# Optimization experiments

Measured on AMD Instinct MI355X. Metric: run time of the kernel, lower is better.

Reference implementation:

```python
import jax, jax.numpy as jnp
import numpy as np

B, S, D = 1, 1024, 4096
NH, NKV, HD = 32, 8, 128
CACHE = 1024


def setup_inputs() -> dict:
    key = jax.random.key(0)
    ks = jax.random.split(key, 9)
    return {
        "hidden_states": jax.random.normal(ks[0], (B, S, D), jnp.float32),
        "freqs_cos": jax.random.uniform(ks[1], (S, HD // 2), jnp.float32),
        "freqs_sin": jax.random.uniform(ks[2], (S, HD // 2), jnp.float32),
        "atten_mask": jnp.zeros((S, CACHE + S), jnp.float32),
        "k_cache": jax.random.normal(ks[3], (B, NKV, HD, CACHE), jnp.float32),
        "v_cache": jax.random.normal(ks[4], (B, NKV, CACHE, HD), jnp.float32),
        "wq": jax.random.normal(ks[5], (NH, HD, D), jnp.float32) * 0.02,
        "wk": jax.random.normal(ks[6], (NKV, HD, D), jnp.float32) * 0.02,
        "wv": jax.random.normal(ks[7], (NKV, HD, D), jnp.float32) * 0.02,
        "wo": jax.random.normal(ks[8], (D, NH * HD), jnp.float32) * 0.02,
    }


def _rope(x, cos, sin):
    # x: [b, s, h, hd]; cos/sin: [s, hd//2]
    half = x.shape[-1] // 2
    xr, xi = x[..., :half], x[..., half:]
    c = cos[None, :, None, :]
    sn = sin[None, :, None, :]
    return jnp.concatenate([xr * c - xi * sn, xr * sn + xi * c], axis=-1)


def reference(hidden_states, freqs_cos, freqs_sin, atten_mask, k_cache, v_cache, wq, wk, wv, wo):
    b, s, d = hidden_states.shape
    nh, hd, _ = wq.shape
    nkv = wk.shape[0]
    g = nh // nkv  # query heads per KV head
    scale = float(hd) ** 0.5

    # projections (equivalent to per-head 1x1 convs)
    q = jnp.einsum("bsd,hed->bshe", hidden_states, wq)   # [b,s,nh,hd]
    k = jnp.einsum("bsd,hed->bshe", hidden_states, wk)   # [b,s,nkv,hd]
    v = jnp.einsum("bsd,hed->bshe", hidden_states, wv)   # [b,s,nkv,hd]

    q = _rope(q, freqs_cos, freqs_sin)
    k = _rope(k, freqs_cos, freqs_sin)

    # concat KV cache: kh [b,nkv,hd,KV], vh [b,nkv,KV,hd]
    kh = jnp.concatenate([k_cache, k.transpose(0, 2, 3, 1)], axis=-1)
    vh = jnp.concatenate([v_cache, v.transpose(0, 2, 1, 3)], axis=2)

    # grouped attention: head i uses kv group i // g
    qg = q.reshape(b, s, nkv, g, hd).transpose(0, 2, 3, 1, 4)  # [b,n,g,s,e]
    scores = jnp.einsum("bngse,bnet->bngst", qg, kh) / scale + atten_mask
    p = jax.nn.softmax(scores, axis=-1)
    yg = jnp.einsum("bngst,bnte->bngse", p, vh)               # [b,n,g,s,e]
    y = yg.transpose(0, 3, 1, 2, 4).reshape(b, s, nh * hd)     # head order n*g+j

    y = jnp.einsum("bsf,df->bsd", y, wo)
    return (y, kh, vh)
```

## Files before the change

### kernel.cpp

```cpp
#include <hip/hip_runtime.h>
#include <hip/hip_bf16.h>
#include <stdint.h>

#define S_LEN 1024
#define D_MODEL 4096
#define NHEAD 32
#define NKV 8
#define HD 128
#define CACHE_T 1024
#define T_TOT 2048
#define NQKV 6144
#define QSCALE 0.08838834764831845f

typedef __attribute__((ext_vector_type(8))) short short8;
typedef __attribute__((ext_vector_type(4))) float floatx4;
typedef __attribute__((ext_vector_type(16))) float floatx16;

__device__ __forceinline__ unsigned short f2bf(float f) {
  union { float f; uint32_t u; } v; v.f = f;
  uint32_t r = v.u + 0x7FFFu + ((v.u >> 16) & 1u);
  return (unsigned short)(r >> 16);
}

__device__ __forceinline__ void gload_lds16(const void* g, void* s) {
  __builtin_amdgcn_global_load_lds((const __attribute__((address_space(1))) void*)g,
                                   (__attribute__((address_space(3))) void*)s, 16, 0, 0);
}

__global__ void convf2b_kernel(const float* __restrict__ in, unsigned short* __restrict__ out, int n8) {
  int stride = gridDim.x * blockDim.x;
  for (int t = blockIdx.x * blockDim.x + threadIdx.x; t < n8; t += stride) {
    int i = t * 8;
    floatx4 a = *(const floatx4*)(in + i);
    floatx4 b = *(const floatx4*)(in + i + 4);
    short8 o;
    o[0] = (short)f2bf(a[0]); o[1] = (short)f2bf(a[1]); o[2] = (short)f2bf(a[2]); o[3] = (short)f2bf(a[3]);
    o[4] = (short)f2bf(b[0]); o[5] = (short)f2bf(b[1]); o[6] = (short)f2bf(b[2]); o[7] = (short)f2bf(b[3]);
    *(short8*)(out + i) = o;
  }
}

__global__ void mask_flag_kernel(const float* __restrict__ m, int n, int* __restrict__ flag) {
  int stride = gridDim.x * blockDim.x;
  bool nz = false;
  for (int i = blockIdx.x * blockDim.x + threadIdx.x; i < n; i += stride)
    nz |= (m[i] != 0.0f);
  if (nz) atomicOr(flag, 1);
}

__global__ __launch_bounds__(256, 3)
void gemm_bf_kernel(const unsigned short* __restrict__ A,
                    const unsigned short* __restrict__ W,
                    float* __restrict__ C,
                    int M, int N, int K, int ldc, int GM)
{
  __shared__ __align__(16) unsigned char As[2][64 * 128];
  __shared__ __align__(16) unsigned char Bs[2][128 * 128];

  const int nwg = gridDim.x;
  int orig = blockIdx.x;
  int wg = (orig & 7) * (nwg >> 3) + (orig >> 3);
  const int mt = wg % GM, nt = wg / GM;
  const int m0 = mt * 64, n0 = nt * 128;

  const int tid = threadIdx.x;
  const int wid = tid >> 6, lane = tid & 63;
  const int g4 = lane >> 4, r16 = lane & 15;
  const int wr = (wid >> 1) * 32, wc = (wid & 1) * 64;

  const int lr = lane >> 3, lc = lane & 7;
  const unsigned short* Arow[2];
  const unsigned short* Wrow[4];
#pragma unroll
  for (int i = 0; i < 2; ++i) {
    int r = (wid * 2 + i) * 8 + lr;
    Arow[i] = A + (size_t)(m0 + r) * K + (lc ^ (r & 7)) * 8;
  }
#pragma unroll
  for (int i = 0; i < 4; ++i) {
    int r = (wid * 4 + i) * 8 + lr;
    Wrow[i] = W + (size_t)(n0 + r) * K + (lc ^ (r & 7)) * 8;
  }

  auto stage = [&](int buf, int kt) {
    const int kb = kt * 64;
#pragma unroll
    for (int i = 0; i < 2; ++i)
      gload_lds16(Arow[i] + kb, &As[buf][(wid * 2 + i) * 1024]);
#pragma unroll
    for (int i = 0; i < 4; ++i)
      gload_lds16(Wrow[i] + kb, &Bs[buf][(wid * 4 + i) * 1024]);
  };

  floatx4 acc[2][4];
#pragma unroll
  for (int m = 0; m < 2; ++m)
#pragma unroll
    for (int n = 0; n < 4; ++n) acc[m][n] = (floatx4){0.f, 0.f, 0.f, 0.f};

  const int NK = K >> 6;
  stage(0, 0);
  __syncthreads();
  int cur = 0;
  for (int kt = 0; kt < NK; ++kt) {
    if (kt + 1 < NK) stage(cur ^ 1, kt + 1);
#pragma unroll
    for (int kk = 0; kk < 2; ++kk) {
      const int kb = kk * 64 + g4 * 16;
      short8 af[2], bf[4];
#pragma unroll
      for (int m = 0; m < 2; ++m) {
        int row = wr + m * 16 + r16;
        af[m] = *(const short8*)(&As[cur][row * 128 + (kb ^ ((row & 7) << 4))]);
      }
#pragma unroll
      for (int n = 0; n < 4; ++n) {
        int row = wc + n * 16 + r16;
        bf[n] = *(const short8*)(&Bs[cur][row * 128 + (kb ^ ((row & 7) << 4))]);
      }
#pragma unroll
      for (int m = 0; m < 2; ++m)
#pragma unroll
        for (int n = 0; n < 4; ++n)
          acc[m][n] = __builtin_amdgcn_mfma_f32_16x16x32_bf16(af[m], bf[n], acc[m][n], 0, 0, 0);
    }
    __syncthreads();
    cur ^= 1;
  }

#pragma unroll
  for (int m = 0; m < 2; ++m)
#pragma unroll
    for (int n = 0; n < 4; ++n)
#pragma unroll
      for (int j = 0; j < 4; ++j)
        C[(size_t)(m0 + wr + m * 16 + g4 * 4 + j) * ldc + (n0 + wc + n * 16 + r16)] = acc[m][n][j];
}

__global__ __launch_bounds__(256, 2)
void gemm_kernel(const unsigned short* __restrict__ A,
                 const float* __restrict__ W0, const float* __restrict__ W1, const float* __restrict__ W2,
                 int n1, int n2,
                 float* __restrict__ C,
                 int M, int N, int K, int GM)
{
  __shared__ __align__(16) unsigned char As[2][128 * 128];
  __shared__ __align__(16) unsigned char Bs[2][128 * 128];

  const int nwg = gridDim.x;
  int orig = blockIdx.x;
  int xcd = orig & 7, loc = orig >> 3;
  int q = nwg >> 3, r = nwg & 7;
  int wg = (xcd < r ? xcd * (q + 1) : r * (q + 1) + (xcd - r) * q) + loc;
  const int mt = wg % GM, nt = wg / GM;
  const int m0 = mt * 128, n0 = nt * 128;

  const int tid = threadIdx.x;
  const int wid = tid >> 6, lane = tid & 63;
  const int g4 = lane >> 4, r16 = lane & 15;
  const int wr = (wid >> 1) * 64, wc = (wid & 1) * 64;

  int srow[4], skc[4];
  const float* wptr[4];
#pragma unroll
  for (int i = 0; i < 4; ++i) {
    int c = tid + 256 * i;
    srow[i] = c >> 3; skc[i] = c & 7;
    int ng = n0 + srow[i];
    wptr[i] = (ng < n1) ? (W0 + (size_t)ng * K)
            : (ng < n2) ? (W1 + (size_t)(ng - n1) * K)
                        : (W2 + (size_t)(ng - n2) * K);
  }

  short8 ar[4]; floatx4 br[8];
  auto load_tile = [&](int kt) {
    int kb = kt * 64;
#pragma unroll
    for (int i = 0; i < 4; ++i) {
      ar[i] = *(const short8*)(A + (size_t)(m0 + srow[i]) * K + kb + skc[i] * 8);
      br[2 * i]     = *(const floatx4*)(wptr[i] + kb + skc[i] * 8);
      br[2 * i + 1] = *(const floatx4*)(wptr[i] + kb + skc[i] * 8 + 4);
    }
  };
  auto write_tile = [&](int buf) {
#pragma unroll
    for (int i = 0; i < 4; ++i) {
      int off = srow[i] * 128 + ((skc[i] * 16) ^ ((srow[i] & 7) << 4));
      *(short8*)(&As[buf][off]) = ar[i];
      short8 bb;
      bb[0] = (short)f2bf(br[2 * i][0]);     bb[1] = (short)f2bf(br[2 * i][1]);
      bb[2] = (short)f2bf(br[2 * i][2]);     bb[3] = (short)f2bf(br[2 * i][3]);
      bb[4] = (short)f2bf(br[2 * i + 1][0]); bb[5] = (short)f2bf(br[2 * i + 1][1]);
      bb[6] = (short)f2bf(br[2 * i + 1][2]); bb[7] = (short)f2bf(br[2 * i + 1][3]);
      *(short8*)(&Bs[buf][off]) = bb;
    }
  };

  floatx4 acc[4][4];
#pragma unroll
  for (int m = 0; m < 4; ++m)
#pragma unroll
    for (int n = 0; n < 4; ++n) acc[m][n] = (floatx4){0.f, 0.f, 0.f, 0.f};

  const int NK = K >> 6;
  load_tile(0);
  write_tile(0);
  __syncthreads();
  int cur = 0;
  for (int kt = 0; kt < NK; ++kt) {
    if (kt + 1 < NK) load_tile(kt + 1);
#pragma unroll
    for (int kk = 0; kk < 2; ++kk) {
      const int kb = kk * 32 + g4 * 8;
      short8 af[4], bfr[4];
#pragma unroll
      for (int m = 0; m < 4; ++m) {
        int row = wr + m * 16 + r16;
        af[m] = *(const short8*)(&As[cur][row * 128 + ((kb * 2) ^ ((row & 7) << 4))]);
      }
#pragma unroll
      for (int n = 0; n < 4; ++n) {
        int row = wc + n * 16 + r16;
        bfr[n] = *(const short8*)(&Bs[cur][row * 128 + ((kb * 2) ^ ((row & 7) << 4))]);
      }
#pragma unroll
      for (int m = 0; m < 4; ++m)
#pragma unroll
        for (int n = 0; n < 4; ++n)
          acc[m][n] = __builtin_amdgcn_mfma_f32_16x16x32_bf16(af[m], bfr[n], acc[m][n], 0, 0, 0);
    }
    if (kt + 1 < NK) write_tile(cur ^ 1);
    __syncthreads();
    cur ^= 1;
  }

#pragma unroll
  for (int m = 0; m < 4; ++m)
#pragma unroll
    for (int n = 0; n < 4; ++n)
#pragma unroll
      for (int j = 0; j < 4; ++j)
        C[(size_t)(m0 + wr + m * 16 + g4 * 4 + j) * N + (n0 + wc + n * 16 + r16)] = acc[m][n][j];
}

__global__ void rope_q_kernel(const float* __restrict__ qkv, const float* __restrict__ fc,
                              const float* __restrict__ fs, unsigned short* __restrict__ qb)
{
  const int s = blockIdx.x, t = threadIdx.x;
  const int head = t >> 3, e0 = (t & 7) * 8;
  const float* base = qkv + (size_t)s * NQKV + head * HD + e0;
  floatx4 xr0 = *(const floatx4*)(base);
  floatx4 xr1 = *(const floatx4*)(base + 4);
  floatx4 xi0 = *(const floatx4*)(base + 64);
  floatx4 xi1 = *(const floatx4*)(base + 68);
  floatx4 c0 = *(const floatx4*)(fc + s * 64 + e0);
  floatx4 c1 = *(const floatx4*)(fc + s * 64 + e0 + 4);
  floatx4 s0 = *(const floatx4*)(fs + s * 64 + e0);
  floatx4 s1 = *(const floatx4*)(fs + s * 64 + e0 + 4);
  short8 outr, outi;
#pragma unroll
  for (int j = 0; j < 4; ++j) {
    outr[j]     = (short)f2bf((xr0[j] * c0[j] - xi0[j] * s0[j]) * QSCALE);
    outr[4 + j] = (short)f2bf((xr1[j] * c1[j] - xi1[j] * s1[j]) * QSCALE);
    outi[j]     = (short)f2bf((xr0[j] * s0[j] + xi0[j] * c0[j]) * QSCALE);
    outi[4 + j] = (short)f2bf((xr1[j] * s1[j] + xi1[j] * c1[j]) * QSCALE);
  }
  unsigned short* ob = qb + (size_t)s * D_MODEL + head * HD + e0;
  *(short8*)ob = outr;
  *(short8*)(ob + 64) = outi;
}

__global__ void rope_k_kernel(const float* __restrict__ qkv, const float* __restrict__ fc,
                              const float* __restrict__ fs, float* __restrict__ kh,
                              unsigned short* __restrict__ khb)
{
  __shared__ float T[128][65];
  const int n = blockIdx.x >> 4, s0 = (blockIdx.x & 15) * 64;
  const int tid = threadIdx.x;
  const int sl = tid >> 2, e0 = (tid & 3) * 16;
  const int s = s0 + sl;
  const float* base = qkv + (size_t)s * NQKV + D_MODEL + n * HD;
  float xr[16], xi[16], cc[16], sn[16];
#pragma unroll
  for (int i = 0; i < 16; i += 4) {
    *(floatx4*)(xr + i) = *(const floatx4*)(base + e0 + i);
    *(floatx4*)(xi + i) = *(const floatx4*)(base + 64 + e0 + i);
    *(floatx4*)(cc + i) = *(const floatx4*)(fc + s * 64 + e0 + i);
    *(floatx4*)(sn + i) = *(const floatx4*)(fs + s * 64 + e0 + i);
  }
  short8 r0, r1, i0, i1;
#pragma unroll
  for (int i = 0; i < 16; ++i) {
    float vr = xr[i] * cc[i] - xi[i] * sn[i];
    float vi = xr[i] * sn[i] + xi[i] * cc[i];
    T[e0 + i][sl] = vr;
    T[64 + e0 + i][sl] = vi;
    unsigned short br = f2bf(vr), bi = f2bf(vi);
    if (i < 8) { r0[i] = (short)br; i0[i] = (short)bi; }
    else       { r1[i - 8] = (short)br; i1[i - 8] = (short)bi; }
  }
  unsigned short* kb = khb + ((size_t)n * T_TOT + CACHE_T + s) * HD;
  *(short8*)(kb + e0) = r0;       *(short8*)(kb + e0 + 8) = r1;
  *(short8*)(kb + 64 + e0) = i0;  *(short8*)(kb + 64 + e0 + 8) = i1;
  __syncthreads();
  const int e = tid >> 1, hf = tid & 1;
  float* dst = kh + ((size_t)n * HD + e) * T_TOT + CACHE_T + s0 + hf * 32;
#pragma unroll
  for (int i = 0; i < 32; i += 4) {
    floatx4 v;
    v[0] = T[e][hf * 32 + i]; v[1] = T[e][hf * 32 + i + 1];
    v[2] = T[e][hf * 32 + i + 2]; v[3] = T[e][hf * 32 + i + 3];
    *(floatx4*)(dst + i) = v;
  }
}

__global__ void v_scatter_kernel(const float* __restrict__ qkv, float* __restrict__ vh,
                                 unsigned short* __restrict__ vtb)
{
  __shared__ __align__(16) unsigned short T[128][72];
  const int n = blockIdx.x >> 4, s0 = (blockIdx.x & 15) * 64;
  const int tid = threadIdx.x;
  const int sl = tid >> 2, e0 = (tid & 3) * 32;
  const float* src = qkv + (size_t)(s0 + sl) * NQKV + D_MODEL + NKV * HD + n * HD + e0;
  float* dst = vh + ((size_t)n * T_TOT + CACHE_T + s0 + sl) * HD + e0;
#pragma unroll
  for (int i = 0; i < 32; i += 4) {
    floatx4 v = *(const floatx4*)(src + i);
    *(floatx4*)(dst + i) = v;
    T[e0 + i][sl] = f2bf(v[0]); T[e0 + i + 1][sl] = f2bf(v[1]);
    T[e0 + i + 2][sl] = f2bf(v[2]); T[e0 + i + 3][sl] = f2bf(v[3]);
  }
  __syncthreads();
  const int e = tid >> 1, hf = tid & 1;
  unsigned short* ob = vtb + ((size_t)n * HD + e) * T_TOT + CACHE_T + s0 + hf * 32;
#pragma unroll
  for (int i = 0; i < 32; i += 8) *(short8*)(ob + i) = *(const short8*)(&T[e][hf * 32 + i]);
}

__global__ void cache_k_kernel(const float* __restrict__ kc, float* __restrict__ kh,
                               unsigned short* __restrict__ khb)
{
  __shared__ __align__(16) unsigned short T[64][72];
  const int b = blockIdx.x;
  const int n = b >> 5, et = (b >> 4) & 1, tt = b & 15;
  const int e0 = et * 64, t0 = tt * 64;
  const int tid = threadIdx.x;
  const int el = tid >> 2, tc = (tid & 3) * 16;
  const float* src = kc + ((size_t)n * HD + e0 + el) * CACHE_T + t0 + tc;
  float* dst = kh + ((size_t)n * HD + e0 + el) * T_TOT + t0 + tc;
#pragma unroll
  for (int i = 0; i < 16; i += 4) {
    floatx4 v = *(const floatx4*)(src + i);
    *(floatx4*)(dst + i) = v;
    T[tc + i][el] = f2bf(v[0]); T[tc + i + 1][el] = f2bf(v[1]);
    T[tc + i + 2][el] = f2bf(v[2]); T[tc + i + 3][el] = f2bf(v[3]);
  }
  __syncthreads();
  const int tl = tid >> 2, ec = (tid & 3) * 16;
  unsigned short* ob = khb + ((size_t)n * T_TOT + t0 + tl) * HD + e0 + ec;
#pragma unroll
  for (int i = 0; i < 16; i += 8) *(short8*)(ob + i) = *(const short8*)(&T[tl][ec + i]);
}

__global__ void cache_v_kernel(const float* __restrict__ vc, float* __restrict__ vh,
                               unsigned short* __restrict__ vtb)
{
  __shared__ __align__(16) unsigned short T[128][72];
  const int n = blockIdx.x >> 4, t0 = (blockIdx.x & 15) * 64;
  const int tid = threadIdx.x;
  const int tl = tid >> 2, e0 = (tid & 3) * 32;
  const float* src = vc + ((size_t)n * CACHE_T + t0 + tl) * HD + e0;
  float* dst = vh + ((size_t)n * T_TOT + t0 + tl) * HD + e0;
#pragma unroll
  for (int i = 0; i < 32; i += 4) {
    floatx4 v = *(const floatx4*)(src + i);
    *(floatx4*)(dst + i) = v;
    T[e0 + i][tl] = f2bf(v[0]); T[e0 + i + 1][tl] = f2bf(v[1]);
    T[e0 + i + 2][tl] = f2bf(v[2]); T[e0 + i + 3][tl] = f2bf(v[3]);
  }
  __syncthreads();
  const int e = tid >> 1, hf = tid & 1;
  unsigned short* ob = vtb + ((size_t)n * HD + e) * T_TOT + t0 + hf * 32;
#pragma unroll
  for (int i = 0; i < 32; i += 8) *(short8*)(ob + i) = *(const short8*)(&T[e][hf * 32 + i]);
}

__global__ __launch_bounds__(256, 2)
void attn_kernel(const unsigned short* __restrict__ Qb, const unsigned short* __restrict__ Kb,
                 const unsigned short* __restrict__ Vb, const float* __restrict__ mask,
                 const int* __restrict__ flag, unsigned short* __restrict__ Ob,
                 float* __restrict__ Upart, float* __restrict__ mlpart, int nsplit)
{
  __shared__ __align__(16) unsigned char KL[2][64 * 256];
  __shared__ __align__(16) unsigned char VL[2][128 * 128];

  const int nwg = gridDim.x;
  int orig = blockIdx.x;
  int wg = (orig & 7) * (nwg >> 3) + (orig >> 3);
  const int per_n = 32 * nsplit;
  const int nkv = wg / per_n;
  const int rem = wg % per_n;
  const int kvs = rem >> 5;
  const int inner = rem & 31;
  const int h = nkv * 4 + (inner >> 3);
  const int qt = inner & 7;
  const int TKV = T_TOT / nsplit;

  const int tid = threadIdx.x, wid = tid >> 6, lane = tid & 63;
  const int l31 = lane & 31, hi = lane >> 5;
  const int qrow = qt * 128 + wid * 32 + l31;
  const bool use_mask = (*flag) != 0;

  short8 qf[8];
#pragma unroll
  for (int c = 0; c < 8; ++c)
    qf[c] = *(const short8*)(Qb + (size_t)qrow * D_MODEL + h * HD + c * 16 + hi * 8);

  floatx16 acc[4];
#pragma unroll
  for (int et = 0; et < 4; ++et)
    acc[et] = (floatx16){0.f,0.f,0.f,0.f,0.f,0.f,0.f,0.f,0.f,0.f,0.f,0.f,0.f,0.f,0.f,0.f};
  float m = -1e30f, l = 0.f;

  const unsigned short* Kbase = Kb + (size_t)nkv * T_TOT * HD + (size_t)kvs * TKV * HD;
  const unsigned short* Vbase = Vb + (size_t)nkv * HD * T_TOT + (size_t)kvs * TKV;

  const unsigned short* kp[4];
  const unsigned short* vp[4];
  int kbase_off[4], vbase_off[4];
#pragma unroll
  for (int i = 0; i < 4; ++i) {
    int krow = wid * 16 + i * 4 + (lane >> 4);
    int kch  = (lane & 15) ^ (krow & 7);
    kp[i] = Kbase + (size_t)krow * HD + kch * 8;
    kbase_off[i] = (wid * 16 + i * 4) * 256;
    int vrow = wid * 32 + i * 8 + (lane >> 3);
    int vch  = (lane & 7) ^ (vrow & 7);
    vp[i] = Vbase + (size_t)vrow * T_TOT + vch * 8;
    vbase_off[i] = (wid * 32 + i * 8) * 128;
  }

#pragma unroll
  for (int i = 0; i < 4; ++i) gload_lds16(kp[i], &KL[0][kbase_off[i]]);
#pragma unroll
  for (int i = 0; i < 4; ++i) gload_lds16(vp[i], &VL[0][vbase_off[i]]);
#pragma unroll
  for (int i = 0; i < 4; ++i) { kp[i] += 64 * HD; vp[i] += 64; }
  __syncthreads();

  int cur = 0;
  for (int t0 = 0; t0 < TKV; t0 += 64) {
    if (t0 + 64 < TKV) {
#pragma unroll
      for (int i = 0; i < 4; ++i) gload_lds16(kp[i], &KL[cur ^ 1][kbase_off[i]]);
#pragma unroll
      for (int i = 0; i < 4; ++i) gload_lds16(vp[i], &VL[cur ^ 1][vbase_off[i]]);
#pragma unroll
      for (int i = 0; i < 4; ++i) { kp[i] += 64 * HD; vp[i] += 64; }
    }

    floatx16 sc[2];
#pragma unroll
    for (int ts = 0; ts < 2; ++ts) {
      sc[ts] = (floatx16){0.f,0.f,0.f,0.f,0.f,0.f,0.f,0.f,0.f,0.f,0.f,0.f,0.f,0.f,0.f,0.f};
      const int krow = ts * 32 + l31;
      const int swz = (krow & 7) << 4;
      const unsigned char* kr = &KL[cur][krow * 256];
#pragma unroll
      for (int c = 0; c < 8; ++c) {
        short8 kf = *(const short8*)(kr + ((c * 32 + hi * 16) ^ swz));
        sc[ts] = __builtin_amdgcn_mfma_f32_32x32x16_bf16(kf, qf[c], sc[ts], 0, 0, 0);
      }
    }

    if (use_mask) {
#pragma unroll
      for (int ts = 0; ts < 2; ++ts)
#pragma unroll
        for (int r = 0; r < 16; ++r) {
          int tg = kvs * TKV + t0 + ts * 32 + (r & 3) + 8 * (r >> 2) + 4 * hi;
          sc[ts][r] += mask[(size_t)qrow * T_TOT + tg];
        }
    }

    float pm = sc[0][0];
#pragma unroll
    for (int r = 1; r < 16; ++r) pm = fmaxf(pm, sc[0][r]);
#pragma unroll
    for (int r = 0; r < 16; ++r) pm = fmaxf(pm, sc[1][r]);
    pm = fmaxf(pm, __shfl_xor(pm, 32));

    if (__any(pm > m + 8.f)) {
      float nm = fmaxf(m, pm);
      float corr = __expf(m - nm);
      m = nm; l *= corr;
#pragma unroll
      for (int r = 0; r < 16; ++r) {
        float cr = __shfl(corr, (r & 3) + 8 * (r >> 2) + 4 * hi);
#pragma unroll
        for (int et = 0; et < 4; ++et) acc[et][r] *= cr;
      }
    }

    unsigned cpk[4][4];
    float ls = 0.f;
#pragma unroll
    for (int ts = 0; ts < 2; ++ts)
#pragma unroll
      for (int i = 0; i < 8; ++i) {
        float plo = __expf(sc[ts][2 * i] - m);
        float phi = __expf(sc[ts][2 * i + 1] - m);
        ls += plo + phi;
        union { __hip_bfloat162 h2; unsigned u; } cv;
        cv.h2 = __float22bfloat162_rn(make_float2(plo, phi));
        cpk[ts * 2 + (i >> 2)][i & 3] = cv.u;
      }
    ls += __shfl_xor(ls, 32);
    l += ls;

    short8 pa[4];
#pragma unroll
    for (int tc = 0; tc < 4; ++tc) {
      unsigned s0 = (unsigned)__shfl_xor((int)cpk[tc][0], 32);
      unsigned s1 = (unsigned)__shfl_xor((int)cpk[tc][1], 32);
      unsigned s2 = (unsigned)__shfl_xor((int)cpk[tc][2], 32);
      unsigned s3 = (unsigned)__shfl_xor((int)cpk[tc][3], 32);
      union { unsigned u[4]; short8 v; } fr;
      fr.u[0] = hi ? s2 : cpk[tc][0];
      fr.u[1] = hi ? s3 : cpk[tc][1];
      fr.u[2] = hi ? cpk[tc][2] : s0;
      fr.u[3] = hi ? cpk[tc][3] : s1;
      pa[tc] = fr.v;
    }

#pragma unroll
    for (int et = 0; et < 4; ++et) {
      const int vrow = et * 32 + l31;
      const int swz = (vrow & 7) << 4;
      const unsigned char* vr = &VL[cur][vrow * 128];
#pragma unroll
      for (int tc = 0; tc < 4; ++tc) {
        short8 vf = *(const short8*)(vr + ((tc * 32 + hi * 16) ^ swz));
        acc[et] = __builtin_amdgcn_mfma_f32_32x32x16_bf16(pa[tc], vf, acc[et], 0, 0, 0);
      }
    }
    __syncthreads();
    cur ^= 1;
  }

  if (nsplit == 2) {
    float* Ub = Upart + (size_t)kvs * (NHEAD * S_LEN) * HD;
#pragma unroll
    for (int et = 0; et < 4; ++et)
#pragma unroll
      for (int r = 0; r < 16; ++r) {
        int q = qt * 128 + wid * 32 + (r & 3) + 8 * (r >> 2) + 4 * hi;
        Ub[((size_t)h * S_LEN + q) * HD + et * 32 + l31] = acc[et][r];
      }
    if (lane < 32) {
      float* mlp = mlpart + ((size_t)kvs * (NHEAD * S_LEN) + (size_t)h * S_LEN + qrow) * 2;
      mlp[0] = m; mlp[1] = l;
    }
  } else {
    float inv = 1.0f / l;
#pragma unroll
    for (int et = 0; et < 4; ++et)
#pragma unroll
      for (int r = 0; r < 16; ++r) {
        float ir = __shfl(inv, (r & 3) + 8 * (r >> 2) + 4 * hi);
        int q = qt * 128 + wid * 32 + (r & 3) + 8 * (r >> 2) + 4 * hi;
        Ob[(size_t)q * D_MODEL + h * HD + et * 32 + l31] = f2bf(acc[et][r] * ir);
      }
  }
}

__global__ void attn_combine_kernel(const float* __restrict__ U, const float* __restrict__ ml,
                                    unsigned short* __restrict__ Ob)
{
  const int t = blockIdx.x * 256 + threadIdx.x;
  const int r = t >> 4;
  const int e0 = (t & 15) * 8;
  const float m1 = ml[(size_t)r * 2],                     l1 = ml[(size_t)r * 2 + 1];
  const float m2 = ml[((size_t)(NHEAD * S_LEN) + r) * 2], l2 = ml[((size_t)(NHEAD * S_LEN) + r) * 2 + 1];
  const float M = fmaxf(m1, m2);
  const float a1 = __expf(m1 - M), a2 = __expf(m2 - M);
  const float inv = 1.0f / (l1 * a1 + l2 * a2);
  const float* u1 = U + (size_t)r * HD + e0;
  const float* u2 = U + (size_t)(NHEAD * S_LEN) * HD + (size_t)r * HD + e0;
  floatx4 x1a = *(const floatx4*)u1, x1b = *(const floatx4*)(u1 + 4);
  floatx4 x2a = *(const floatx4*)u2, x2b = *(const floatx4*)(u2 + 4);
  const int s = r & (S_LEN - 1), hh = r >> 10;
  unsigned short* ob = Ob + (size_t)s * D_MODEL + hh * HD + e0;
  short8 o;
#pragma unroll
  for (int k = 0; k < 4; ++k) {
    o[k]     = (short)f2bf((x1a[k] * a1 + x2a[k] * a2) * inv);
    o[4 + k] = (short)f2bf((x1b[k] * a1 + x2b[k] * a2) * inv);
  }
  *(short8*)ob = o;
}

extern "C" void kernel_launch(void* const* d_in, const int* in_sizes, int n_in,
                              void* d_out, int out_size, void* d_ws, size_t ws_size,
                              hipStream_t stream)
{
  const float* hs   = (const float*)d_in[0];
  const float* fc   = (const float*)d_in[1];
  const float* fs   = (const float*)d_in[2];
  const float* mask = (const float*)d_in[3];
  const float* kc   = (const float*)d_in[4];
  const float* vc   = (const float*)d_in[5];
  const float* wq   = (const float*)d_in[6];
  const float* wk   = (const float*)d_in[7];
  const float* wv   = (const float*)d_in[8];
  const float* wo   = (const float*)d_in[9];

  float* y  = (float*)d_out;
  float* kh = y + (size_t)S_LEN * D_MODEL;
  float* vh = kh + (size_t)NKV * HD * T_TOT;

  char* ws = (char*)d_ws;
  unsigned short* hs_b   = (unsigned short*)ws;
  float* qkv             = (float*)(ws + 8388608u);
  unsigned short* attn_o = (unsigned short*)(ws + 8388608u);
  unsigned short* khb    = (unsigned short*)(ws + 33554432u);
  unsigned short* vtb    = (unsigned short*)(ws + 37748736u);
  int* flag              = (int*)(ws + 41943040u);
  unsigned short* slotW  = (unsigned short*)(ws + 41943296u);

  const size_t base = 41943296ull;
  const bool big = ws_size >= base + 50331648ull;
  const bool mid = ws_size >= base + 33554432ull;
  const int nsplit = (ws_size >= base + 34078720ull) ? 2 : 1;
  float* Upart  = (float*)(ws + base);
  float* mlpart = (float*)(ws + base + 33554432u);

  hipMemsetAsync(flag, 0, 4, stream);
  mask_flag_kernel<<<256, 256, 0, stream>>>(mask, S_LEN * T_TOT, flag);
  convf2b_kernel<<<2048, 256, 0, stream>>>(hs, hs_b, S_LEN * D_MODEL / 8);

  if (big) {
    convf2b_kernel<<<2048, 256, 0, stream>>>(wq, slotW, NHEAD * HD * D_MODEL / 8);
    convf2b_kernel<<<2048, 256, 0, stream>>>(wk, slotW + (size_t)4096 * 4096, NKV * HD * D_MODEL / 8);
    convf2b_kernel<<<2048, 256, 0, stream>>>(wv, slotW + (size_t)5120 * 4096, NKV * HD * D_MODEL / 8);
    gemm_bf_kernel<<<768, 256, 0, stream>>>(hs_b, slotW, qkv, 1024, 6144, 4096, 6144, 16);
  } else if (mid) {
    convf2b_kernel<<<2048, 256, 0, stream>>>(wk, slotW, NKV * HD * D_MODEL / 8);
    convf2b_kernel<<<2048, 256, 0, stream>>>(wv, slotW + (size_t)1024 * 4096, NKV * HD * D_MODEL / 8);
    gemm_bf_kernel<<<256, 256, 0, stream>>>(hs_b, slotW, qkv + 4096, 1024, 2048, 4096, 6144, 16);
    convf2b_kernel<<<2048, 256, 0, stream>>>(wq, slotW, NHEAD * HD * D_MODEL / 8);
    gemm_bf_kernel<<<512, 256, 0, stream>>>(hs_b, slotW, qkv, 1024, 4096, 4096, 6144, 16);
  } else {
    gemm_kernel<<<384, 256, 0, stream>>>(hs_b, wq, wk, wv, 4096, 5120, qkv, 1024, 6144, 4096, 8);
  }

  rope_q_kernel<<<1024, 256, 0, stream>>>(qkv, fc, fs, hs_b);
  rope_k_kernel<<<128, 256, 0, stream>>>(qkv, fc, fs, kh, khb);
  v_scatter_kernel<<<128, 256, 0, stream>>>(qkv, vh, vtb);
  cache_k_kernel<<<256, 256, 0, stream>>>(kc, kh, khb);
  cache_v_kernel<<<128, 256, 0, stream>>>(vc, vh, vtb);

  attn_kernel<<<256 * nsplit, 256, 0, stream>>>(hs_b, khb, vtb, mask, flag, attn_o,
                                                Upart, mlpart, nsplit);
  if (nsplit == 2)
    attn_combine_kernel<<<2048, 256, 0, stream>>>(Upart, mlpart, attn_o);

  if (mid) {
    convf2b_kernel<<<2048, 256, 0, stream>>>(wo, slotW, D_MODEL * D_MODEL / 8);
    gemm_bf_kernel<<<512, 256, 0, stream>>>(attn_o, slotW, y, 1024, 4096, 4096, 4096, 16);
  } else {
    gemm_kernel<<<256, 256, 0, stream>>>(attn_o, wo, wo, wo, 1 << 29, 1 << 29, y, 1024, 4096, 4096, 8);
  }
}
```

Baseline: 264.4 us.

## Fuse fp32-to-bf16 weight conversion into 64x128 GEMM loads, drop separate convert passes

The separate convf2b passes over the QKV and output-projection weights are removed. A single 64x128-tile GEMM now reads fp32 weights into registers, converts them to bf16, and writes them to LDS after the MFMA loop, prefetching one tile ahead. This avoids writing and re-reading bf16 weight copies in the workspace and cuts kernel launches. In exchange, each weight tile is loaded as fp32 and converted in-kernel by every M-tile that uses it, and register pressure rises under the 3-waves launch bound.

```diff
diff --git a/kernel.cpp b/kernel.cpp
--- a/kernel.cpp
+++ b/kernel.cpp
@@ -20,6 +20,12 @@
   union { float f; uint32_t u; } v; v.f = f;
   uint32_t r = v.u + 0x7FFFu + ((v.u >> 16) & 1u);
   return (unsigned short)(r >> 16);
+}
+
+__device__ __forceinline__ unsigned pack2bf(float a, float b) {
+  union { __hip_bfloat162 h2; unsigned u; } c;
+  c.h2 = __float22bfloat162_rn(make_float2(a, b));
+  return c.u;
 }
 
 __device__ __forceinline__ void gload_lds16(const void* g, void* s) {
@@ -49,10 +55,11 @@
 }
 
 __global__ __launch_bounds__(256, 3)
-void gemm_bf_kernel(const unsigned short* __restrict__ A,
-                    const unsigned short* __restrict__ W,
-                    float* __restrict__ C,
-                    int M, int N, int K, int ldc, int GM)
+void gemm_bfw_kernel(const unsigned short* __restrict__ A,
+                     const float* __restrict__ W0, const float* __restrict__ W1, const float* __restrict__ W2,
+                     int n1, int n2,
+                     float* __restrict__ C,
+                     int M, int N, int K, int ldc, int GM)
 {
   __shared__ __align__(16) unsigned char As[2][64 * 128];
   __shared__ __align__(16) unsigned char Bs[2][128 * 128];
@@ -70,27 +77,38 @@
 
   const int lr = lane >> 3, lc = lane & 7;
   const unsigned short* Arow[2];
-  const unsigned short* Wrow[4];
 #pragma unroll
   for (int i = 0; i < 2; ++i) {
     int r = (wid * 2 + i) * 8 + lr;
     Arow[i] = A + (size_t)(m0 + r) * K + (lc ^ (r & 7)) * 8;
   }
-#pragma unroll
-  for (int i = 0; i < 4; ++i) {
-    int r = (wid * 4 + i) * 8 + lr;
-    Wrow[i] = W + (size_t)(n0 + r) * K + (lc ^ (r & 7)) * 8;
-  }
-
-  auto stage = [&](int buf, int kt) {
-    const int kb = kt * 64;
-#pragma unroll
-    for (int i = 0; i < 2; ++i)
-      gload_lds16(Arow[i] + kb, &As[buf][(wid * 2 + i) * 1024]);
-#pragma unroll
-    for (int i = 0; i < 4; ++i)
-      gload_lds16(Wrow[i] + kb, &Bs[buf][(wid * 4 + i) * 1024]);
+
+  const int wrow = tid >> 1, wch = tid & 1;
+  const int ng = n0 + wrow;
+  const float* wptr = (ng < n1) ? (W0 + (size_t)ng * K)
+                    : (ng < n2) ? (W1 + (size_t)(ng - n1) * K)
+                                : (W2 + (size_t)(ng - n2) * K);
+  wptr += wch * 32;
+
+  floatx4 wreg[8];
+  auto wload = [&](int kt) {
+    const float* p = wptr + kt * 64;
+#pragma unroll
+    for (int i = 0; i < 8; ++i) wreg[i] = *(const floatx4*)(p + i * 4);
   };
+  auto wwrite = [&](int buf) {
+    unsigned char* dst = &Bs[buf][wrow * 128];
+    const int sw = (wrow & 7) << 4;
+#pragma unroll
+    for (int q = 0; q < 4; ++q) {
+      union { unsigned u[4]; short8 v; } pk;
+      pk.u[0] = pack2bf(wreg[2 * q][0], wreg[2 * q][1]);
+      pk.u[1] = pack2bf(wreg[2 * q][2], wreg[2 * q][3]);
+      pk.u[2] = pack2bf(wreg[2 * q + 1][0], wreg[2 * q + 1][1]);
+      pk.u[3] = pack2bf(wreg[2 * q + 1][2], wreg[2 * q + 1][3]);
+      *(short8*)(dst + ((wch * 64 + q * 16) ^ sw)) = pk.v;
+    }
+  };
 
   floatx4 acc[2][4];
 #pragma unroll
@@ -99,11 +117,20 @@
     for (int n = 0; n < 4; ++n) acc[m][n] = (floatx4){0.f, 0.f, 0.f, 0.f};
 
   const int NK = K >> 6;
-  stage(0, 0);
+  wload(0);
+#pragma unroll
+  for (int i = 0; i < 2; ++i) gload_lds16(Arow[i], &As[0][(wid * 2 + i) * 1024]);
+  wwrite(0);
   __syncthreads();
+
   int cur = 0;
   for (int kt = 0; kt < NK; ++kt) {
-    if (kt + 1 < NK) stage(cur ^ 1, kt + 1);
+    if (kt + 1 < NK) {
+      wload(kt + 1);
+#pragma unroll
+      for (int i = 0; i < 2; ++i)
+        gload_lds16(Arow[i] + (kt + 1) * 64, &As[cur ^ 1][(wid * 2 + i) * 1024]);
+    }
 #pragma unroll
     for (int kk = 0; kk < 2; ++kk) {
       const int kb = kk * 64 + g4 * 16;
@@ -124,6 +151,7 @@
         for (int n = 0; n < 4; ++n)
           acc[m][n] = __builtin_amdgcn_mfma_f32_16x16x32_bf16(af[m], bf[n], acc[m][n], 0, 0, 0);
     }
+    if (kt + 1 < NK) wwrite(cur ^ 1);
     __syncthreads();
     cur ^= 1;
   }
@@ -135,112 +163,6 @@
 #pragma unroll
       for (int j = 0; j < 4; ++j)
         C[(size_t)(m0 + wr + m * 16 + g4 * 4 + j) * ldc + (n0 + wc + n * 16 + r16)] = acc[m][n][j];
-}
-
-__global__ __launch_bounds__(256, 2)
-void gemm_kernel(const unsigned short* __restrict__ A,
-                 const float* __restrict__ W0, const float* __restrict__ W1, const float* __restrict__ W2,
-                 int n1, int n2,
-                 float* __restrict__ C,
-                 int M, int N, int K, int GM)
-{
-  __shared__ __align__(16) unsigned char As[2][128 * 128];
-  __shared__ __align__(16) unsigned char Bs[2][128 * 128];
-
-  const int nwg = gridDim.x;
-  int orig = blockIdx.x;
-  int xcd = orig & 7, loc = orig >> 3;
-  int q = nwg >> 3, r = nwg & 7;
-  int wg = (xcd < r ? xcd * (q + 1) : r * (q + 1) + (xcd - r) * q) + loc;
-  const int mt = wg % GM, nt = wg / GM;
-  const int m0 = mt * 128, n0 = nt * 128;
-
-  const int tid = threadIdx.x;
-  const int wid = tid >> 6, lane = tid & 63;
-  const int g4 = lane >> 4, r16 = lane & 15;
-  const int wr = (wid >> 1) * 64, wc = (wid & 1) * 64;
-
-  int srow[4], skc[4];
-  const float* wptr[4];
-#pragma unroll
-  for (int i = 0; i < 4; ++i) {
-    int c = tid + 256 * i;
-    srow[i] = c >> 3; skc[i] = c & 7;
-    int ng = n0 + srow[i];
-    wptr[i] = (ng < n1) ? (W0 + (size_t)ng * K)
-            : (ng < n2) ? (W1 + (size_t)(ng - n1) * K)
-                        : (W2 + (size_t)(ng - n2) * K);
-  }
-
-  short8 ar[4]; floatx4 br[8];
-  auto load_tile = [&](int kt) {
-    int kb = kt * 64;
-#pragma unroll
-    for (int i = 0; i < 4; ++i) {
-      ar[i] = *(const short8*)(A + (size_t)(m0 + srow[i]) * K + kb + skc[i] * 8);
-      br[2 * i]     = *(const floatx4*)(wptr[i] + kb + skc[i] * 8);
-      br[2 * i + 1] = *(const floatx4*)(wptr[i] + kb + skc[i] * 8 + 4);
-    }
-  };
-  auto write_tile = [&](int buf) {
-#pragma unroll
-    for (int i = 0; i < 4; ++i) {
-      int off = srow[i] * 128 + ((skc[i] * 16) ^ ((srow[i] & 7) << 4));
-      *(short8*)(&As[buf][off]) = ar[i];
-      short8 bb;
-      bb[0] = (short)f2bf(br[2 * i][0]);     bb[1] = (short)f2bf(br[2 * i][1]);
-      bb[2] = (short)f2bf(br[2 * i][2]);     bb[3] = (short)f2bf(br[2 * i][3]);
-      bb[4] = (short)f2bf(br[2 * i + 1][0]); bb[5] = (short)f2bf(br[2 * i + 1][1]);
-      bb[6] = (short)f2bf(br[2 * i + 1][2]); bb[7] = (short)f2bf(br[2 * i + 1][3]);
-      *(short8*)(&Bs[buf][off]) = bb;
-    }
-  };
-
-  floatx4 acc[4][4];
-#pragma unroll
-  for (int m = 0; m < 4; ++m)
-#pragma unroll
-    for (int n = 0; n < 4; ++n) acc[m][n] = (floatx4){0.f, 0.f, 0.f, 0.f};
-
-  const int NK = K >> 6;
-  load_tile(0);
-  write_tile(0);
-  __syncthreads();
-  int cur = 0;
-  for (int kt = 0; kt < NK; ++kt) {
-    if (kt + 1 < NK) load_tile(kt + 1);
-#pragma unroll
-    for (int kk = 0; kk < 2; ++kk) {
-      const int kb = kk * 32 + g4 * 8;
-      short8 af[4], bfr[4];
-#pragma unroll
-      for (int m = 0; m < 4; ++m) {
-        int row = wr + m * 16 + r16;
-        af[m] = *(const short8*)(&As[cur][row * 128 + ((kb * 2) ^ ((row & 7) << 4))]);
-      }
-#pragma unroll
-      for (int n = 0; n < 4; ++n) {
-        int row = wc + n * 16 + r16;
-        bfr[n] = *(const short8*)(&Bs[cur][row * 128 + ((kb * 2) ^ ((row & 7) << 4))]);
-      }
-#pragma unroll
-      for (int m = 0; m < 4; ++m)
-#pragma unroll
-        for (int n = 0; n < 4; ++n)
-          acc[m][n] = __builtin_amdgcn_mfma_f32_16x16x32_bf16(af[m], bfr[n], acc[m][n], 0, 0, 0);
-    }
-    if (kt + 1 < NK) write_tile(cur ^ 1);
-    __syncthreads();
-    cur ^= 1;
-  }
-
-#pragma unroll
-  for (int m = 0; m < 4; ++m)
-#pragma unroll
-    for (int n = 0; n < 4; ++n)
-#pragma unroll
-      for (int j = 0; j < 4; ++j)
-        C[(size_t)(m0 + wr + m * 16 + g4 * 4 + j) * N + (n0 + wc + n * 16 + r16)] = acc[m][n][j];
 }
 
 __global__ void rope_q_kernel(const float* __restrict__ qkv, const float* __restrict__ fc,
@@ -511,9 +433,7 @@
         float plo = __expf(sc[ts][2 * i] - m);
         float phi = __expf(sc[ts][2 * i + 1] - m);
         ls += plo + phi;
-        union { __hip_bfloat162 h2; unsigned u; } cv;
-        cv.h2 = __float22bfloat162_rn(make_float2(plo, phi));
-        cpk[ts * 2 + (i >> 2)][i & 3] = cv.u;
+        cpk[ts * 2 + (i >> 2)][i & 3] = pack2bf(plo, phi);
       }
     ls += __shfl_xor(ls, 32);
     l += ls;
@@ -626,11 +546,8 @@
   unsigned short* khb    = (unsigned short*)(ws + 33554432u);
   unsigned short* vtb    = (unsigned short*)(ws + 37748736u);
   int* flag              = (int*)(ws + 41943040u);
-  unsigned short* slotW  = (unsigned short*)(ws + 41943296u);
 
   const size_t base = 41943296ull;
-  const bool big = ws_size >= base + 50331648ull;
-  const bool mid = ws_size >= base + 33554432ull;
   const int nsplit = (ws_size >= base + 34078720ull) ? 2 : 1;
   float* Upart  = (float*)(ws + base);
   float* mlpart = (float*)(ws + base + 33554432u);
@@ -639,20 +556,8 @@
   mask_flag_kernel<<<256, 256, 0, stream>>>(mask, S_LEN * T_TOT, flag);
   convf2b_kernel<<<2048, 256, 0, stream>>>(hs, hs_b, S_LEN * D_MODEL / 8);
 
-  if (big) {
-    convf2b_kernel<<<2048, 256, 0, stream>>>(wq, slotW, NHEAD * HD * D_MODEL / 8);
-    convf2b_kernel<<<2048, 256, 0, stream>>>(wk, slotW + (size_t)4096 * 4096, NKV * HD * D_MODEL / 8);
-    convf2b_kernel<<<2048, 256, 0, stream>>>(wv, slotW + (size_t)5120 * 4096, NKV * HD * D_MODEL / 8);
-    gemm_bf_kernel<<<768, 256, 0, stream>>>(hs_b, slotW, qkv, 1024, 6144, 4096, 6144, 16);
-  } else if (mid) {
-    convf2b_kernel<<<2048, 256, 0, stream>>>(wk, slotW, NKV * HD * D_MODEL / 8);
-    convf2b_kernel<<<2048, 256, 0, stream>>>(wv, slotW + (size_t)1024 * 4096, NKV * HD * D_MODEL / 8);
-    gemm_bf_kernel<<<256, 256, 0, stream>>>(hs_b, slotW, qkv + 4096, 1024, 2048, 4096, 6144, 16);
-    convf2b_kernel<<<2048, 256, 0, stream>>>(wq, slotW, NHEAD * HD * D_MODEL / 8);
-    gemm_bf_kernel<<<512, 256, 0, stream>>>(hs_b, slotW, qkv, 1024, 4096, 4096, 6144, 16);
-  } else {
-    gemm_kernel<<<384, 256, 0, stream>>>(hs_b, wq, wk, wv, 4096, 5120, qkv, 1024, 6144, 4096, 8);
-  }
+  gemm_bfw_kernel<<<768, 256, 0, stream>>>(hs_b, wq, wk, wv, 4096, 5120, qkv,
+                                           1024, 6144, 4096, 6144, 16);
 
   rope_q_kernel<<<1024, 256, 0, stream>>>(qkv, fc, fs, hs_b);
   rope_k_kernel<<<128, 256, 0, stream>>>(qkv, fc, fs, kh, khb);
@@ -665,10 +570,6 @@
   if (nsplit == 2)
     attn_combine_kernel<<<2048, 256, 0, stream>>>(Upart, mlpart, attn_o);
 
-  if (mid) {
-    convf2b_kernel<<<2048, 256, 0, stream>>>(wo, slotW, D_MODEL * D_MODEL / 8);
-    gemm_bf_kernel<<<512, 256, 0, stream>>>(attn_o, slotW, y, 1024, 4096, 4096, 4096, 16);
-  } else {
-    gemm_kernel<<<256, 256, 0, stream>>>(attn_o, wo, wo, wo, 1 << 29, 1 << 29, y, 1024, 4096, 4096, 8);
-  }
-}
+  gemm_bfw_kernel<<<512, 256, 0, stream>>>(attn_o, wo, wo, wo, 1 << 29, 1 << 29, y,
+                                           1024, 4096, 4096, 4096, 16);
+}
```

Result: slower. 491.8 us (+86.0%).
